# Kernel tuning notes

Measured on AMD Instinct MI355X. Metric: run time of the kernel, lower is better.

Reference implementation:

```python
import jax, jax.numpy as jnp
import numpy as np

RES_LIST = [16, 32, 64, 128]
N_DIMS = 3
N_FIELDS = 4
N_POINTS = 2_000_000


def _value_noise(x, V, res, mult):
    """One ValueNoise level: trilinear interpolation of grid V at points x.

    x: [N, n_dims] float, V: [(res+1),]*n_dims + [n_fields], smoothness=2.
    """
    n_dims = x.shape[1]
    xs = jnp.fmod(x * res, res)                      # [N, d]
    fl = jnp.floor(xs)
    locs = xs - fl                                   # frac part, [N, d]
    ia = fl.astype(jnp.int32)                        # floor index
    ib = ia + 1                                      # non-periodic: grid has res+1 nodes
    idx = jnp.stack((ia, ib), axis=-1)               # [N, d, 2]
    corners = jnp.indices((2,) * n_dims)             # [d, 2,2,2]
    # per-dim corner indices, each [N, 2,2,2]
    gather_idx = tuple(idx[:, i, :][:, corners[i]] for i in range(n_dims))
    vals = V[gather_idx]                             # [N, 2,2,2, n_fields]
    # smoothness=2 fade: w = (3 - 2w) w^2
    w = (3.0 - 2.0 * locs) * locs * locs             # [N, d]
    for i in range(n_dims):
        wi = w[:, i].reshape((-1,) + (1,) * (n_dims - i))
        a, b = vals[:, 0], vals[:, 1]
        vals = a + wi * (b - a)                      # lerp along dim i
    return vals * mult                               # [N, n_fields]


def setup_inputs() -> dict:
    key = jax.random.key(0)
    kx, k0, k1, k2, k3 = jax.random.split(key, 5)
    x = jax.random.uniform(kx, (N_POINTS, N_DIMS), dtype=jnp.float32)
    grids = {}
    for k, res in zip((k0, k1, k2, k3), RES_LIST):
        grids[f"V{res}"] = jax.random.normal(
            k, (res + 1,) * N_DIMS + (N_FIELDS,), dtype=jnp.float32)
    return {"x": x, **grids}


def reference(x, V16, V32, V64, V128):
    grids = (V16, V32, V64, V128)
    out = jnp.zeros((x.shape[0], N_FIELDS), dtype=x.dtype)
    for V, res in zip(grids, RES_LIST):
        mult = float(RES_LIST[0]) / float(res)       # multiplier * res_list[0]/res
        out = out + _value_noise(x, V, res, mult)
    return out
```

## Files before the change

### kernel.cpp

```cpp
#include <hip/hip_runtime.h>
#include <hip/hip_fp16.h>


#define NB 1024
#define PTS_PER_BLK 4096
#define CHUNK 32
#define SC_THREADS 1024
#define SC_PPT (PTS_PER_BLK / SC_THREADS)
#define H_THREADS 256
#define H_PPT (PTS_PER_BLK / H_THREADS)
#define MT 512

__device__ __forceinline__ int bucket_of(float px, float py, float pz) {
    int ix = min(max((int)(px * 16.0f), 0), 15);
    int iy = min(max((int)(py * 8.0f), 0), 7);
    int iz = min(max((int)(pz * 8.0f), 0), 7);
    return (ix * 8 + iy) * 8 + iz;
}

__global__ void __launch_bounds__(H_THREADS)
cvn_hist(const float* __restrict__ x, int* __restrict__ P, int n) {
    __shared__ int cnt[NB];
    int t = threadIdx.x;
    for (int q = t; q < NB; q += H_THREADS) cnt[q] = 0;
    __syncthreads();
    int base = blockIdx.x * PTS_PER_BLK;
    for (int k = 0; k < H_PPT; ++k) {
        int i = base + k * H_THREADS + t;
        if (i < n)
            atomicAdd(&cnt[bucket_of(x[3 * i], x[3 * i + 1], x[3 * i + 2])], 1);
    }
    __syncthreads();
    int* Pb = P + (size_t)blockIdx.x * NB;
    for (int q = t; q < NB; q += H_THREADS) Pb[q] = cnt[q];
}

__global__ void __launch_bounds__(256)
cvn_scan_a(const int* __restrict__ P, int* __restrict__ S, int nblk) {
    int q = blockIdx.x * 256 + threadIdx.x;
    int c = blockIdx.y;
    int b0 = c * CHUNK, b1 = min(b0 + CHUNK, nblk);
    int s = 0;
    for (int b = b0; b < b1; ++b) s += P[(size_t)b * NB + q];
    S[(size_t)c * NB + q] = s;
}

__global__ void __launch_bounds__(NB)
cvn_scan_b(int* __restrict__ S, int nch) {
    __shared__ int part[16];
    int t = threadIdx.x;
    int lane = t & 63, wid = t >> 6;
    int acc = 0;
    for (int c = 0; c < nch; ++c) {
        int v = S[(size_t)c * NB + t];
        S[(size_t)c * NB + t] = acc;
        acc += v;
    }
    int sum = acc;
    #pragma unroll
    for (int off = 1; off < 64; off <<= 1) {
        int v = __shfl_up(sum, off, 64);
        if (lane >= off) sum += v;
    }
    if (lane == 63) part[wid] = sum;
    __syncthreads();
    if (t < 16) {
        int p = part[t];
        int s2 = p;
        #pragma unroll
        for (int off = 1; off < 16; off <<= 1) {
            int v = __shfl_up(s2, off, 64);
            if (t >= off) s2 += v;
        }
        part[t] = s2 - p;
    }
    __syncthreads();
    int texcl = part[wid] + (sum - acc);
    for (int c = 0; c < nch; ++c) S[(size_t)c * NB + t] += texcl;
}

__global__ void __launch_bounds__(256)
cvn_scan_c(int* __restrict__ P, const int* __restrict__ S, int nblk) {
    int q = blockIdx.x * 256 + threadIdx.x;
    int c = blockIdx.y;
    int b0 = c * CHUNK, b1 = min(b0 + CHUNK, nblk);
    int run = S[(size_t)c * NB + q];
    for (int b = b0; b < b1; ++b) {
        int v = P[(size_t)b * NB + q];
        P[(size_t)b * NB + q] = run;
        run += v;
    }
}

__global__ void __launch_bounds__(SC_THREADS)
cvn_scatter(const float* __restrict__ x, const int* __restrict__ P,
            float4* __restrict__ sorted, int n) {
    __shared__ int cnt[NB];
    __shared__ int place[NB];
    __shared__ int Pb[NB];
    __shared__ int sc[NB];
    __shared__ float4 payload[PTS_PER_BLK];
    __shared__ unsigned short bkt[PTS_PER_BLK];
    int t = threadIdx.x, b = blockIdx.x;
    int base = b * PTS_PER_BLK;
    cnt[t] = 0; place[t] = 0;
    Pb[t] = P[(size_t)b * NB + t];
    __syncthreads();

    float px[SC_PPT], py[SC_PPT], pz[SC_PPT];
    int qq[SC_PPT];
    #pragma unroll
    for (int k = 0; k < SC_PPT; ++k) {
        int i = base + k * SC_THREADS + t;
        if (i < n) {
            px[k] = x[3 * i]; py[k] = x[3 * i + 1]; pz[k] = x[3 * i + 2];
            qq[k] = bucket_of(px[k], py[k], pz[k]);
            atomicAdd(&cnt[qq[k]], 1);
        } else qq[k] = -1;
    }
    __syncthreads();

    sc[t] = cnt[t];
    __syncthreads();
    for (int off = 1; off < NB; off <<= 1) {
        int v = (t >= off) ? sc[t - off] : 0;
        __syncthreads();
        if (t >= off) sc[t] += v;
        __syncthreads();
    }
    cnt[t] = (t == 0) ? 0 : sc[t - 1];
    __syncthreads();

    #pragma unroll
    for (int k = 0; k < SC_PPT; ++k) {
        if (qq[k] >= 0) {
            int q = qq[k];
            int lp = atomicAdd(&place[q], 1);
            int slot = cnt[q] + lp;
            int i = base + k * SC_THREADS + t;
            payload[slot] = make_float4(px[k], py[k], pz[k], __int_as_float(i));
            bkt[slot] = (unsigned short)q;
        }
    }
    __syncthreads();

    int total = min(n - base, PTS_PER_BLK);
    #pragma unroll
    for (int k = 0; k < SC_PPT; ++k) {
        int j = k * SC_THREADS + t;
        if (j < total) {
            int q = bkt[j];
            sorted[Pb[q] + (j - cnt[q])] = payload[j];
        }
    }
}

__device__ __forceinline__ float4 lerp4(float4 a, float4 b, float w) {
    return make_float4(a.x + w * (b.x - a.x),
                       a.y + w * (b.y - a.y),
                       a.z + w * (b.z - a.z),
                       a.w + w * (b.w - a.w));
}

template <int RES>
__device__ __forceinline__ float4 level_val(const float4* __restrict__ V,
                                            float px, float py, float pz) {
    constexpr int S = RES + 1;
    float xs = fmodf(px * (float)RES, (float)RES);
    float ys = fmodf(py * (float)RES, (float)RES);
    float zs = fmodf(pz * (float)RES, (float)RES);
    float fx = floorf(xs), fy = floorf(ys), fz = floorf(zs);
    float tx = xs - fx, ty = ys - fy, tz = zs - fz;
    int ix = (int)fx, iy = (int)fy, iz = (int)fz;

    float wx = (3.0f - 2.0f * tx) * tx * tx;
    float wy = (3.0f - 2.0f * ty) * ty * ty;
    float wz = (3.0f - 2.0f * tz) * tz * tz;

    int base = (ix * S + iy) * S + iz;
    const float4* p0 = V + base;
    const float4* p1 = p0 + S * S;

    float4 c000 = p0[0];
    float4 c001 = p0[1];
    float4 c010 = p0[S];
    float4 c011 = p0[S + 1];
    float4 c100 = p1[0];
    float4 c101 = p1[1];
    float4 c110 = p1[S];
    float4 c111 = p1[S + 1];

    float4 m00 = lerp4(c000, c100, wx);
    float4 m01 = lerp4(c001, c101, wx);
    float4 m10 = lerp4(c010, c110, wx);
    float4 m11 = lerp4(c011, c111, wx);
    float4 n0  = lerp4(m00, m10, wy);
    float4 n1  = lerp4(m01, m11, wy);
    return lerp4(n0, n1, wz);
}

__device__ __forceinline__ float4 composite(const float4* __restrict__ V16,
                                            const float4* __restrict__ V32,
                                            const float4* __restrict__ V64,
                                            const float4* __restrict__ V128,
                                            float px, float py, float pz) {
    float4 acc = level_val<16>(V16, px, py, pz);
    float4 v;
    v = level_val<32>(V32, px, py, pz);
    acc.x += 0.5f * v.x; acc.y += 0.5f * v.y; acc.z += 0.5f * v.z; acc.w += 0.5f * v.w;
    v = level_val<64>(V64, px, py, pz);
    acc.x += 0.25f * v.x; acc.y += 0.25f * v.y; acc.z += 0.25f * v.z; acc.w += 0.25f * v.w;
    v = level_val<128>(V128, px, py, pz);
    acc.x += 0.125f * v.x; acc.y += 0.125f * v.y; acc.z += 0.125f * v.z; acc.w += 0.125f * v.w;
    return acc;
}

__device__ __forceinline__ float4 ldh4(const uint2* p) {
    uint2 u = *p;
    __half2 h0 = *reinterpret_cast<const __half2*>(&u.x);
    __half2 h1 = *reinterpret_cast<const __half2*>(&u.y);
    float2 f0 = __half22float2(h0);
    float2 f1 = __half22float2(h1);
    return make_float4(f0.x, f0.y, f1.x, f1.y);
}

__device__ __forceinline__ uint2 sth4(float4 v) {
    __half2 h0 = __floats2half2_rn(v.x, v.y);
    __half2 h1 = __floats2half2_rn(v.z, v.w);
    uint2 u;
    u.x = *reinterpret_cast<unsigned int*>(&h0);
    u.y = *reinterpret_cast<unsigned int*>(&h1);
    return u;
}

template <int RES>
__device__ __forceinline__ float4 lds_interp_h(const uint2* s,
                                               float px, float py, float pz,
                                               int ix16, int iy8, int iz8) {
    constexpr int CX = RES / 16, CY = RES / 8, CZ = RES / 8;
    constexpr int DY = CY + 1, DZ = CZ + 1;
    float xs = px * (float)RES;
    float ys = py * (float)RES;
    float zs = pz * (float)RES;
    int ixg = (int)xs, iyg = (int)ys, izg = (int)zs;
    float tx = xs - (float)ixg, ty = ys - (float)iyg, tz = zs - (float)izg;
    int lx = min(max(ixg - ix16 * CX, 0), CX - 1);
    int ly = min(max(iyg - iy8 * CY, 0), CY - 1);
    int lz = min(max(izg - iz8 * CZ, 0), CZ - 1);

    float wx = (3.0f - 2.0f * tx) * tx * tx;
    float wy = (3.0f - 2.0f * ty) * ty * ty;
    float wz = (3.0f - 2.0f * tz) * tz * tz;

    const uint2* p0 = s + (lx * DY + ly) * DZ + lz;
    const uint2* p1 = p0 + DY * DZ;
    float4 c000 = ldh4(p0),      c001 = ldh4(p0 + 1);
    float4 c010 = ldh4(p0 + DZ), c011 = ldh4(p0 + DZ + 1);
    float4 c100 = ldh4(p1),      c101 = ldh4(p1 + 1);
    float4 c110 = ldh4(p1 + DZ), c111 = ldh4(p1 + DZ + 1);

    float4 m00 = lerp4(c000, c100, wx);
    float4 m01 = lerp4(c001, c101, wx);
    float4 m10 = lerp4(c010, c110, wx);
    float4 m11 = lerp4(c011, c111, wx);
    float4 n0  = lerp4(m00, m10, wy);
    float4 n1  = lerp4(m01, m11, wy);
    return lerp4(n0, n1, wz);
}

__global__ void __launch_bounds__(MT, 8)
cvn_main4(const float4* __restrict__ sorted, const int* __restrict__ Tbase,
          const float4* __restrict__ V16, const float4* __restrict__ V32,
          const float4* __restrict__ V64, const float4* __restrict__ V128,
          float4* __restrict__ out, int n) {
    __shared__ uint2 s128[9 * 17 * 17];
    __shared__ uint2 s64[5 * 9 * 9];
    int t = threadIdx.x, b = blockIdx.x;

    int ox = b & 1, oy = (b >> 1) & 1, oz = (b >> 2) & 1;
    int g  = b >> 3;
    int gx = g >> 4, gy = (g >> 2) & 3, gz = g & 3;
    int ix16 = ox * 8 + gx, iy8 = oy * 4 + gy, iz8 = oz * 4 + gz;
    int q = (ix16 * 8 + iy8) * 8 + iz8;

    int base = Tbase[q];
    int end  = (q == NB - 1) ? n : Tbase[q + 1];
    int len  = end - base;

    int bx = ix16 * 8, by = iy8 * 16, bz = iz8 * 16;
    for (int u = t; u < 2601; u += MT) {
        int a = u / 289, r = u - a * 289;
        int bb = r / 17, c = r - bb * 17;
        s128[u] = sth4(V128[((size_t)(bx + a) * 129 + (by + bb)) * 129
                            + (bz + c)]);
    }
    for (int u = t; u < 405; u += MT) {
        int a = u / 81, r = u - a * 81;
        int bb = r / 9, c = r - bb * 9;
        s64[u] = sth4(V64[((size_t)(ix16 * 4 + a) * 65 + (iy8 * 8 + bb)) * 65
                          + (iz8 * 8 + c)]);
    }
    __syncthreads();

    for (int p = t; p < len; p += MT) {
        float4 pt = sorted[base + p];
        float4 acc = level_val<16>(V16, pt.x, pt.y, pt.z);
        float4 v;
        v = level_val<32>(V32, pt.x, pt.y, pt.z);
        acc.x += 0.5f * v.x; acc.y += 0.5f * v.y;
        acc.z += 0.5f * v.z; acc.w += 0.5f * v.w;
        v = lds_interp_h<64>(s64, pt.x, pt.y, pt.z, ix16, iy8, iz8);
        acc.x += 0.25f * v.x; acc.y += 0.25f * v.y;
        acc.z += 0.25f * v.z; acc.w += 0.25f * v.w;
        v = lds_interp_h<128>(s128, pt.x, pt.y, pt.z, ix16, iy8, iz8);
        acc.x += 0.125f * v.x; acc.y += 0.125f * v.y;
        acc.z += 0.125f * v.z; acc.w += 0.125f * v.w;
        out[__float_as_int(pt.w)] = acc;
    }
}

__global__ void __launch_bounds__(256)
cvn_direct(const float* __restrict__ x,
           const float4* __restrict__ V16, const float4* __restrict__ V32,
           const float4* __restrict__ V64, const float4* __restrict__ V128,
           float4* __restrict__ out, int n) {
    int i = blockIdx.x * blockDim.x + threadIdx.x;
    if (i >= n) return;
    out[i] = composite(V16, V32, V64, V128, x[3 * i], x[3 * i + 1], x[3 * i + 2]);
}

extern "C" void kernel_launch(void* const* d_in, const int* in_sizes, int n_in,
                              void* d_out, int out_size, void* d_ws, size_t ws_size,
                              hipStream_t stream) {
    const float*  x    = (const float*)d_in[0];
    const float4* V16  = (const float4*)d_in[1];
    const float4* V32  = (const float4*)d_in[2];
    const float4* V64  = (const float4*)d_in[3];
    const float4* V128 = (const float4*)d_in[4];
    float4* out = (float4*)d_out;

    int n = in_sizes[0] / 3;
    int nblk = (n + PTS_PER_BLK - 1) / PTS_PER_BLK;
    int nch  = (nblk + CHUNK - 1) / CHUNK;

    auto align256 = [](size_t v) { return (v + 255) & ~(size_t)255; };
    size_t offP      = 0;
    size_t offS      = align256(offP + (size_t)nblk * NB * sizeof(int));
    size_t offSorted = align256(offS + (size_t)nch * NB * sizeof(int));
    size_t need      = offSorted + (size_t)n * sizeof(float4);

    int grid256 = (n + 255) / 256;

    if (ws_size >= need) {
        int*    P      = (int*)((char*)d_ws + offP);
        int*    S      = (int*)((char*)d_ws + offS);
        float4* sorted = (float4*)((char*)d_ws + offSorted);

        cvn_hist<<<nblk, H_THREADS, 0, stream>>>(x, P, n);
        cvn_scan_a<<<dim3(NB / 256, nch), 256, 0, stream>>>(P, S, nblk);
        cvn_scan_b<<<1, NB, 0, stream>>>(S, nch);
        cvn_scan_c<<<dim3(NB / 256, nch), 256, 0, stream>>>(P, S, nblk);
        cvn_scatter<<<nblk, SC_THREADS, 0, stream>>>(x, P, sorted, n);
        cvn_main4<<<NB, MT, 0, stream>>>(sorted, S, V16, V32, V64, V128,
                                         out, n);
    } else {
        cvn_direct<<<grid256, 256, 0, stream>>>(x, V16, V32, V64, V128, out, n);
    }
}
```

Before: 187.9 us.

## Fuse chunk sums into histogram, use wave-shuffle scan, stage coarse grids in LDS

The histogram kernel now atomically adds its per-block bucket counts into per-chunk sums, which removes the separate scan_a pass. A memset is added to zero those sums first. The block-local exclusive scan in scatter is replaced by a wavefront shuffle scan plus a 16-entry cross-wave scan, cutting many __syncthreads rounds. The main kernel also stages the small res-16 and res-32 grid tiles in LDS as float4 instead of reading them through global gathers.

```diff
diff --git a/kernel.cpp b/kernel.cpp
--- a/kernel.cpp
+++ b/kernel.cpp
@@ -19,7 +19,8 @@
 }
 
 __global__ void __launch_bounds__(H_THREADS)
-cvn_hist(const float* __restrict__ x, int* __restrict__ P, int n) {
+cvn_hist(const float* __restrict__ x, int* __restrict__ P,
+         int* __restrict__ S, int n) {
     __shared__ int cnt[NB];
     int t = threadIdx.x;
     for (int q = t; q < NB; q += H_THREADS) cnt[q] = 0;
@@ -32,17 +33,12 @@
     }
     __syncthreads();
     int* Pb = P + (size_t)blockIdx.x * NB;
-    for (int q = t; q < NB; q += H_THREADS) Pb[q] = cnt[q];
-}
-
-__global__ void __launch_bounds__(256)
-cvn_scan_a(const int* __restrict__ P, int* __restrict__ S, int nblk) {
-    int q = blockIdx.x * 256 + threadIdx.x;
-    int c = blockIdx.y;
-    int b0 = c * CHUNK, b1 = min(b0 + CHUNK, nblk);
-    int s = 0;
-    for (int b = b0; b < b1; ++b) s += P[(size_t)b * NB + q];
-    S[(size_t)c * NB + q] = s;
+    int* Sc = S + (size_t)(blockIdx.x / CHUNK) * NB;
+    for (int q = t; q < NB; q += H_THREADS) {
+        int v = cnt[q];
+        Pb[q] = v;
+        if (v) atomicAdd(&Sc[q], v);
+    }
 }
 
 __global__ void __launch_bounds__(NB)
@@ -98,10 +94,11 @@
     __shared__ int cnt[NB];
     __shared__ int place[NB];
     __shared__ int Pb[NB];
-    __shared__ int sc[NB];
+    __shared__ int part[16];
     __shared__ float4 payload[PTS_PER_BLK];
     __shared__ unsigned short bkt[PTS_PER_BLK];
     int t = threadIdx.x, b = blockIdx.x;
+    int lane = t & 63, wid = t >> 6;
     int base = b * PTS_PER_BLK;
     cnt[t] = 0; place[t] = 0;
     Pb[t] = P[(size_t)b * NB + t];
@@ -120,15 +117,27 @@
     }
     __syncthreads();
 
-    sc[t] = cnt[t];
-    __syncthreads();
-    for (int off = 1; off < NB; off <<= 1) {
-        int v = (t >= off) ? sc[t - off] : 0;
-        __syncthreads();
-        if (t >= off) sc[t] += v;
-        __syncthreads();
-    }
-    cnt[t] = (t == 0) ? 0 : sc[t - 1];
+    int c0 = cnt[t];
+    int sum = c0;
+    #pragma unroll
+    for (int off = 1; off < 64; off <<= 1) {
+        int v = __shfl_up(sum, off, 64);
+        if (lane >= off) sum += v;
+    }
+    if (lane == 63) part[wid] = sum;
+    __syncthreads();
+    if (t < 16) {
+        int p = part[t];
+        int s2 = p;
+        #pragma unroll
+        for (int off = 1; off < 16; off <<= 1) {
+            int v = __shfl_up(s2, off, 64);
+            if (t >= off) s2 += v;
+        }
+        part[t] = s2 - p;
+    }
+    __syncthreads();
+    cnt[t] = part[wid] + (sum - c0);
     __syncthreads();
 
     #pragma unroll
@@ -268,6 +277,41 @@
     return lerp4(n0, n1, wz);
 }
 
+template <int RES>
+__device__ __forceinline__ float4 lds_interp_b(const float4* s,
+                                               float px, float py, float pz,
+                                               int ix16, int iy8, int iz8) {
+    constexpr int CX = RES / 16, CY = RES / 8, CZ = RES / 8;
+    constexpr int DY = CY + 1, DZ = CZ + 1;
+    float xs = px * (float)RES;
+    float ys = py * (float)RES;
+    float zs = pz * (float)RES;
+    int ixg = (int)xs, iyg = (int)ys, izg = (int)zs;
+    float tx = xs - (float)ixg, ty = ys - (float)iyg, tz = zs - (float)izg;
+    int lx = min(max(ixg - ix16 * CX, 0), CX - 1);
+    int ly = min(max(iyg - iy8 * CY, 0), CY - 1);
+    int lz = min(max(izg - iz8 * CZ, 0), CZ - 1);
+
+    float wx = (3.0f - 2.0f * tx) * tx * tx;
+    float wy = (3.0f - 2.0f * ty) * ty * ty;
+    float wz = (3.0f - 2.0f * tz) * tz * tz;
+
+    const float4* p0 = s + (lx * DY + ly) * DZ + lz;
+    const float4* p1 = p0 + DY * DZ;
+    float4 c000 = p0[0],  c001 = p0[1];
+    float4 c010 = p0[DZ], c011 = p0[DZ + 1];
+    float4 c100 = p1[0],  c101 = p1[1];
+    float4 c110 = p1[DZ], c111 = p1[DZ + 1];
+
+    float4 m00 = lerp4(c000, c100, wx);
+    float4 m01 = lerp4(c001, c101, wx);
+    float4 m10 = lerp4(c010, c110, wx);
+    float4 m11 = lerp4(c011, c111, wx);
+    float4 n0  = lerp4(m00, m10, wy);
+    float4 n1  = lerp4(m01, m11, wy);
+    return lerp4(n0, n1, wz);
+}
+
 __global__ void __launch_bounds__(MT, 8)
 cvn_main4(const float4* __restrict__ sorted, const int* __restrict__ Tbase,
           const float4* __restrict__ V16, const float4* __restrict__ V32,
@@ -275,6 +319,8 @@
           float4* __restrict__ out, int n) {
     __shared__ uint2 s128[9 * 17 * 17];
     __shared__ uint2 s64[5 * 9 * 9];
+    __shared__ float4 s32f[3 * 5 * 5];
+    __shared__ float4 s16f[2 * 3 * 3];
     int t = threadIdx.x, b = blockIdx.x;
 
     int ox = b & 1, oy = (b >> 1) & 1, oz = (b >> 2) & 1;
@@ -300,13 +346,25 @@
         s64[u] = sth4(V64[((size_t)(ix16 * 4 + a) * 65 + (iy8 * 8 + bb)) * 65
                           + (iz8 * 8 + c)]);
     }
+    for (int u = t; u < 75; u += MT) {
+        int a = u / 25, r = u - a * 25;
+        int bb = r / 5, c = r - bb * 5;
+        s32f[u] = V32[((size_t)(ix16 * 2 + a) * 33 + (iy8 * 4 + bb)) * 33
+                      + (iz8 * 4 + c)];
+    }
+    for (int u = t; u < 18; u += MT) {
+        int a = u / 9, r = u - a * 9;
+        int bb = r / 3, c = r - bb * 3;
+        s16f[u] = V16[((size_t)(ix16 + a) * 17 + (iy8 * 2 + bb)) * 17
+                      + (iz8 * 2 + c)];
+    }
     __syncthreads();
 
     for (int p = t; p < len; p += MT) {
         float4 pt = sorted[base + p];
-        float4 acc = level_val<16>(V16, pt.x, pt.y, pt.z);
+        float4 acc = lds_interp_b<16>(s16f, pt.x, pt.y, pt.z, ix16, iy8, iz8);
         float4 v;
-        v = level_val<32>(V32, pt.x, pt.y, pt.z);
+        v = lds_interp_b<32>(s32f, pt.x, pt.y, pt.z, ix16, iy8, iz8);
         acc.x += 0.5f * v.x; acc.y += 0.5f * v.y;
         acc.z += 0.5f * v.z; acc.w += 0.5f * v.w;
         v = lds_interp_h<64>(s64, pt.x, pt.y, pt.z, ix16, iy8, iz8);
@@ -356,8 +414,8 @@
         int*    S      = (int*)((char*)d_ws + offS);
         float4* sorted = (float4*)((char*)d_ws + offSorted);
 
-        cvn_hist<<<nblk, H_THREADS, 0, stream>>>(x, P, n);
-        cvn_scan_a<<<dim3(NB / 256, nch), 256, 0, stream>>>(P, S, nblk);
+        hipMemsetAsync(S, 0, (size_t)nch * NB * sizeof(int), stream);
+        cvn_hist<<<nblk, H_THREADS, 0, stream>>>(x, P, S, n);
         cvn_scan_b<<<1, NB, 0, stream>>>(S, nch);
         cvn_scan_c<<<dim3(NB / 256, nch), 256, 0, stream>>>(P, S, nblk);
         cvn_scatter<<<nblk, SC_THREADS, 0, stream>>>(x, P, sorted, n);
```

After: 420.1 us. +123.5%, slower.
